# Optimization experiments

Hardware: AMD Instinct MI355X
Metric: run time of the kernel (lower is better)

The kernel has to match this reference:

```python
import jax, jax.numpy as jnp
import numpy as np

B, C_IN, N, K = 4, 128, 2048, 16
DIM, POS, PH, AH = 256, 3, 64, 256 * 4
EPS = 1e-5


def _conv1x1(x, W, b):
    # 1x1 Conv2d: x (B, Cin, n, k) -> (B, Cout, n, k)
    return jnp.einsum('oc,bcnk->bonk', W, x) + b[None, :, None, None]


def _bn(x, gamma, beta, mean, var):
    # eval-mode BatchNorm2d with running stats
    scale = gamma / jnp.sqrt(var + EPS)
    return x * scale[None, :, None, None] + (beta - mean * scale)[None, :, None, None]


def _forward(key, values, pos, Wk, bk, Wq, bq, Wv, bv,
             Wp1, bp1, pg, pb, pm, pv, Wp2, bp2,
             Wa1, ba1, ag, ab, am, av, Wa2, ba2, We, be):
    b, _, n, k = key.shape
    pos_f = jnp.broadcast_to(pos[:, :, :, None], (b, pos.shape[1], n, k))
    kf = _conv1x1(key, Wk, bk)          # (B, dim, n, k)
    v = _conv1x1(values, Wv, bv)        # (B, dim, n, k)
    q = _conv1x1(pos_f, Wq, bq)         # (B, dim, n, k)
    qk_rel = q - kf
    pe = _conv1x1(jax.nn.relu(_bn(_conv1x1(q, Wp1, bp1), pg, pb, pm, pv)), Wp2, bp2)
    attn = _conv1x1(jax.nn.relu(_bn(_conv1x1(qk_rel * pe + pe, Wa1, ba1), ag, ab, am, av)), Wa2, ba2)
    attn = jax.nn.softmax(attn, axis=-1)  # softmax over k neighbors
    agg = jnp.einsum('bcnk,bcnk->bcn', attn, v + pe)  # (B, dim, n)
    return jnp.einsum('oc,bcn->bon', We, agg) + be[None, :, None]


def setup_inputs():
    ks = jax.random.split(jax.random.key(0), 12)
    s = 0.02
    f32 = jnp.float32
    return {
        'key': jax.random.normal(ks[0], (B, C_IN, N, K), f32),
        'values': jax.random.normal(ks[1], (B, C_IN, N, K), f32),
        'pos': jax.random.normal(ks[2], (B, POS, N), f32),
        'Wk': jax.random.normal(ks[3], (DIM, C_IN), f32) * s,
        'bk': jnp.zeros((DIM,), f32),
        'Wq': jax.random.normal(ks[4], (DIM, POS), f32) * s,
        'bq': jnp.zeros((DIM,), f32),
        'Wv': jax.random.normal(ks[5], (DIM, C_IN), f32) * s,
        'bv': jnp.zeros((DIM,), f32),
        'Wp1': jax.random.normal(ks[6], (PH, DIM), f32) * s,
        'bp1': jnp.zeros((PH,), f32),
        'pg': jnp.ones((PH,), f32),
        'pb': jnp.zeros((PH,), f32),
        'pm': jnp.zeros((PH,), f32),
        'pv': jnp.ones((PH,), f32),
        'Wp2': jax.random.normal(ks[7], (DIM, PH), f32) * s,
        'bp2': jnp.zeros((DIM,), f32),
        'Wa1': jax.random.normal(ks[8], (AH, DIM), f32) * s,
        'ba1': jnp.zeros((AH,), f32),
        'ag': jnp.ones((AH,), f32),
        'ab': jnp.zeros((AH,), f32),
        'am': jnp.zeros((AH,), f32),
        'av': jnp.ones((AH,), f32),
        'Wa2': jax.random.normal(ks[9], (DIM, AH), f32) * s,
        'ba2': jnp.zeros((DIM,), f32),
        'We': jax.random.normal(ks[10], (DIM, DIM), f32) * s,
        'be': jnp.zeros((DIM,), f32),
    }


def reference(key, values, pos, Wk, bk, Wq, bq, Wv, bv,
              Wp1, bp1, pg, pb, pm, pv, Wp2, bp2,
              Wa1, ba1, ag, ab, am, av, Wa2, ba2, We, be):
    return _forward(key, values, pos, Wk, bk, Wq, bq, Wv, bv,
                    Wp1, bp1, pg, pb, pm, pv, Wp2, bp2,
                    Wa1, ba1, ag, ab, am, av, Wa2, ba2, We, be)
```

## Files before the change

kernel.cpp:

```cpp
#include <hip/hip_runtime.h>
#include <math.h>

typedef __attribute__((ext_vector_type(8))) short bf16x8;
typedef __attribute__((ext_vector_type(4))) float f32x4;

namespace {
constexpr int NN = 2048;
constexpr float EPSV = 1e-5f;

constexpr size_t WK_O   = 0;
constexpr size_t WV_O   = 65536;
constexpr size_t WEP_O  = 131072;
constexpr size_t B1F_O  = 262144;
constexpr size_t WIMG_O = 266240;
constexpr size_t WP1Q_O = 1314816;
constexpr size_t SC_O   = 1315840;

constexpr int DBUF_OFF = 0;
constexpr int SCW_OFF  = 32768;
constexpr int PE_OFF   = 40960;
constexpr int B1L_OFF  = 49152;
constexpr int LDS_TOTAL = 53248;
}

__device__ __forceinline__ unsigned short f2bf(float x) {
    unsigned u = __float_as_uint(x);
    unsigned r = (u + 0x7FFFu + ((u >> 16) & 1u)) >> 16;
    return (unsigned short)r;
}
__device__ __forceinline__ float bf2f(unsigned short h) {
    return __uint_as_float(((unsigned)h) << 16);
}
__device__ __forceinline__ void gl_lds16(const void* gsrc, void* ldst) {
    __builtin_amdgcn_global_load_lds(
        (const __attribute__((address_space(1))) unsigned int*)gsrc,
        (__attribute__((address_space(3))) unsigned int*)ldst,
        16, 0, 0);
}


__global__ void prep_sc(const float* __restrict__ ag,  const float* __restrict__ ab,
                        const float* __restrict__ am,  const float* __restrict__ av,
                        const float* __restrict__ ba1,
                        const float* __restrict__ Wp1, const float* __restrict__ Wq,
                        const float* __restrict__ bq,  const float* __restrict__ bp1,
                        const float* __restrict__ pg,  const float* __restrict__ pb,
                        const float* __restrict__ pm,  const float* __restrict__ pv,
                        char* __restrict__ ws)
{
    const int t = threadIdx.x, blk = blockIdx.x;
    float* b1f  = (float*)(ws + B1F_O);
    float* sc_s = (float*)(ws + SC_O);
    float* wp1q = (float*)(ws + WP1Q_O);
    if (blk < 4) {
        int j = blk * 256 + t;
        float sc = ag[j] * rsqrtf(av[j] + EPSV);
        sc_s[j] = sc;
        b1f[j] = ba1[j] * sc + ab[j] - am[j] * sc;
    } else if (t < 64) {
        int ph = t;
        float scp = pg[ph] * rsqrtf(pv[ph] + EPSV);
        float a0 = 0.f, a1 = 0.f, a2 = 0.f, abv = 0.f;
        for (int c = 0; c < 256; ++c) {
            float wv = Wp1[ph * 256 + c];
            a0 = fmaf(wv, Wq[c * 3 + 0], a0);
            a1 = fmaf(wv, Wq[c * 3 + 1], a1);
            a2 = fmaf(wv, Wq[c * 3 + 2], a2);
            abv = fmaf(wv, bq[c], abv);
        }
        wp1q[ph * 4 + 0] = scp * a0;
        wp1q[ph * 4 + 1] = scp * a1;
        wp1q[ph * 4 + 2] = scp * a2;
        wp1q[ph * 4 + 3] = scp * (abv + bp1[ph]) + (pb[ph] - pm[ph] * scp);
    }
}

__global__ void prep_cvt(const float* __restrict__ Wk, const float* __restrict__ Wv,
                         const float* __restrict__ We, const float* __restrict__ Wa1,
                         const float* __restrict__ Wa2, char* __restrict__ ws)
{
    const int idx4 = blockIdx.x * 256 + threadIdx.x;
    if (idx4 >= 163840) return;
    const int e0 = idx4 * 4;
    const float* sc_s = (const float*)(ws + SC_O);

    if (e0 < 131072) {
        const float* src;
        unsigned short* dst;
        if (e0 < 32768)      { src = Wk + e0;          dst = (unsigned short*)(ws + WK_O)  + e0; }
        else if (e0 < 65536) { int e = e0 - 32768; src = Wv + e; dst = (unsigned short*)(ws + WV_O)  + e; }
        else                 { int e = e0 - 65536; src = We + e; dst = (unsigned short*)(ws + WEP_O) + e; }
        float4 v = *(const float4*)src;
        ushort4 o;
        o.x = f2bf(v.x); o.y = f2bf(v.y); o.z = f2bf(v.z); o.w = f2bf(v.w);
        *(ushort4*)dst = o;
    } else if (e0 < 393216) {
        int e = e0 - 131072;
        int j = e >> 8, c = e & 255;
        float sc = sc_s[j];
        float4 v = *(const float4*)(Wa1 + e);
        int p = j >> 5, jl = j & 31;
        size_t byte = (size_t)p * 32768 + ((jl * 512 + c * 2) ^ ((jl & 7) << 4));
        ushort4 o;
        o.x = f2bf(v.x * sc); o.y = f2bf(v.y * sc); o.z = f2bf(v.z * sc); o.w = f2bf(v.w * sc);
        *(ushort4*)(ws + WIMG_O + byte) = o;
    } else {
        int e = e0 - 393216;
        int o = e >> 10, j = e & 1023;
        float4 v = *(const float4*)(Wa2 + e);
        int p = j >> 5, jj = j & 31;
        size_t byte = (size_t)p * 32768 + 16384 +
                      (((o >> 1) * 128 + (o & 1) * 64 + jj * 2) ^ (((o >> 1) & 7) << 4));
        ushort4 ov;
        ov.x = f2bf(v.x); ov.y = f2bf(v.y); ov.z = f2bf(v.z); ov.w = f2bf(v.w);
        *(ushort4*)(ws + WIMG_O + byte) = ov;
    }
}

__global__ __launch_bounds__(256) __attribute__((amdgpu_waves_per_eu(2, 2)))
void pt_main(const float* __restrict__ key, const float* __restrict__ values,
             const float* __restrict__ pos,
             const float* __restrict__ Wq,  const float* __restrict__ bq,
             const float* __restrict__ bk,  const float* __restrict__ bv,
             const float* __restrict__ Wp2, const float* __restrict__ bp2,
             const float* __restrict__ be,
             const char* __restrict__ ws,
             float* __restrict__ outp)
{
    extern __shared__ char sm[];
    const int t = threadIdx.x;
    const int w = t >> 6, l = t & 63;
    const int l15 = l & 15, lg = l >> 4;
    const int wg = (blockIdx.x & 7) * 128 + (blockIdx.x >> 3);
    const int b = wg >> 8;
    const int n0 = (wg & 255) * 8;

    char* scw = sm + SCW_OFF + w * 2048;
    char* pew = sm + PE_OFF + w * 2048;
    float* b1l = (float*)(sm + B1L_OFF);

    const unsigned short* wkp = (const unsigned short*)(ws + WK_O);
    const unsigned short* wvp = (const unsigned short*)(ws + WV_O);
    const unsigned short* wep = (const unsigned short*)(ws + WEP_O);
    const float* b1fp = (const float*)(ws + B1F_O);
    const float* wp1q = (const float*)(ws + WP1Q_O);
    const char* wimg = ws + WIMG_O;

    const f32x4 zf = {0.f, 0.f, 0.f, 0.f};

    #pragma unroll
    for (int i = 0; i < 8; ++i)
        gl_lds16(wimg + i * 4096 + t * 16, sm + DBUF_OFF + i * 4096 + t * 16);

    #pragma unroll
    for (int i = 0; i < 4; ++i) b1l[t + i * 256] = b1fp[t + i * 256];

    float p_[2][3];
    {
        const float4 wq4 = *(const float4*)(wp1q + l * 4);
        float h1v[2];
        #pragma unroll
        for (int nl = 0; nl < 2; ++nl) {
            int n = n0 + 2 * w + nl;
            p_[nl][0] = pos[(b * 3 + 0) * NN + n];
            p_[nl][1] = pos[(b * 3 + 1) * NN + n];
            p_[nl][2] = pos[(b * 3 + 2) * NN + n];
            h1v[nl] = fmaxf(fmaf(wq4.x, p_[nl][0],
                            fmaf(wq4.y, p_[nl][1],
                            fmaf(wq4.z, p_[nl][2], wq4.w))), 0.f);
        }
        float pacc[2][4];
        #pragma unroll
        for (int nl = 0; nl < 2; ++nl)
            #pragma unroll
            for (int oi = 0; oi < 4; ++oi) pacc[nl][oi] = 0.f;
        #pragma unroll 4
        for (int j4 = 0; j4 < 16; ++j4) {
            float h0[4], h1[4];
            #pragma unroll
            for (int jj = 0; jj < 4; ++jj) {
                h0[jj] = __shfl(h1v[0], j4 * 4 + jj);
                h1[jj] = __shfl(h1v[1], j4 * 4 + jj);
            }
            #pragma unroll
            for (int oi = 0; oi < 4; ++oi) {
                const float4 wv4 = *(const float4*)(Wp2 + (oi * 64 + l) * 64 + j4 * 4);
                pacc[0][oi] = fmaf(wv4.x, h0[0], fmaf(wv4.y, h0[1], fmaf(wv4.z, h0[2], fmaf(wv4.w, h0[3], pacc[0][oi]))));
                pacc[1][oi] = fmaf(wv4.x, h1[0], fmaf(wv4.y, h1[1], fmaf(wv4.z, h1[2], fmaf(wv4.w, h1[3], pacc[1][oi]))));
            }
        }
        #pragma unroll
        for (int oi = 0; oi < 4; ++oi) {
            int o = oi * 64 + l;
            float bp = bp2[o], bko = bk[o], bqo = bq[o];
            float wq0 = Wq[o * 3 + 0], wq1 = Wq[o * 3 + 1], wq2 = Wq[o * 3 + 2];
            #pragma unroll
            for (int nl = 0; nl < 2; ++nl) {
                float pe = pacc[nl][oi] + bp;
                float q  = fmaf(wq0, p_[nl][0], fmaf(wq1, p_[nl][1], fmaf(wq2, p_[nl][2], bqo)));
                *(unsigned short*)(pew + nl * 512 + o * 2)        = f2bf((q + 1.f - bko) * pe);
                *(unsigned short*)(pew + 1024 + nl * 512 + o * 2) = f2bf(pe);
            }
        }
    }

    const int kq = l & 3, nv = (l >> 2) & 1, c0 = l >> 3;
    f32x4 kacc[2][16];
    #pragma unroll
    for (int mt = 0; mt < 2; ++mt)
        #pragma unroll
        for (int ot = 0; ot < 16; ++ot) kacc[mt][ot] = zf;

    #pragma unroll 1
    for (int s = 0; s < 4; ++s) {
        const float* kb = key + ((size_t)b * 128 * NN + (size_t)(n0 + 2 * w + nv)) * 16 + kq * 4;
        #pragma unroll
        for (int i = 0; i < 4; ++i) {
            int c = s * 32 + i * 8 + c0;
            float4 v = *(const float4*)(kb + (size_t)c * NN * 16);
            int cl = i * 8 + c0;
            #pragma unroll
            for (int j = 0; j < 4; ++j) {
                int m = nv * 16 + kq * 4 + j;
                float fj = (j == 0) ? v.x : (j == 1) ? v.y : (j == 2) ? v.z : v.w;
                *(unsigned short*)(scw + (((m >> 1) * 128 + (m & 1) * 64 + cl * 2) ^ (((m >> 1) & 7) << 4))) = f2bf(fj);
            }
        }
        bf16x8 kB[2];
        #pragma unroll
        for (int mt = 0; mt < 2; ++mt) {
            int m = mt * 16 + l15;
            kB[mt] = *(const bf16x8*)(scw + (((m >> 1) * 128 + (m & 1) * 64 + lg * 16) ^ (((m >> 1) & 7) << 4)));
        }
        #pragma unroll 4
        for (int ot = 0; ot < 16; ++ot) {
            bf16x8 aW = *(const bf16x8*)(wkp + (ot * 16 + l15) * 128 + s * 32 + lg * 8);
            kacc[0][ot] = __builtin_amdgcn_mfma_f32_16x16x32_bf16(aW, kB[0], kacc[0][ot], 0, 0, 0);
            kacc[1][ot] = __builtin_amdgcn_mfma_f32_16x16x32_bf16(aW, kB[1], kacc[1][ot], 0, 0, 0);
        }
    }

    bf16x8 ax[2][8];
    #pragma unroll 1
    for (int x = 0; x < 8; ++x) {
        #pragma unroll
        for (int mt = 0; mt < 2; ++mt) {
            const int m = mt * 16 + l15;
            #pragma unroll
            for (int oi = 0; oi < 2; ++oi) {
                int ot = x * 2 + oi;
                int o0 = ot * 16 + lg * 4;
                ushort4 qv  = *(const ushort4*)(pew + mt * 512 + o0 * 2);
                ushort4 pv4 = *(const ushort4*)(pew + 1024 + mt * 512 + o0 * 2);
                ushort4 pk;
                pk.x = f2bf(bf2f(qv.x) - kacc[mt][ot][0] * bf2f(pv4.x));
                pk.y = f2bf(bf2f(qv.y) - kacc[mt][ot][1] * bf2f(pv4.y));
                pk.z = f2bf(bf2f(qv.z) - kacc[mt][ot][2] * bf2f(pv4.z));
                pk.w = f2bf(bf2f(qv.w) - kacc[mt][ot][3] * bf2f(pv4.w));
                int ol = oi * 16 + lg * 4;
                *(ushort4*)(scw + (((m >> 1) * 128 + (m & 1) * 64 + ol * 2) ^ (((m >> 1) & 7) << 4))) = pk;
            }
        }
        #pragma unroll
        for (int mt = 0; mt < 2; ++mt) {
            int m = mt * 16 + l15;
            ax[mt][x] = *(const bf16x8*)(scw + (((m >> 1) * 128 + (m & 1) * 64 + lg * 16) ^ (((m >> 1) & 7) << 4)));
        }
    }

    f32x4 Y[2][16];
    #pragma unroll
    for (int mt = 0; mt < 2; ++mt)
        #pragma unroll
        for (int ot = 0; ot < 16; ++ot) Y[mt][ot] = zf;

    char* hrb = scw;

    #pragma unroll 1
    for (int p = 0; p < 32; ++p) {
        asm volatile("s_waitcnt vmcnt(0) lgkmcnt(0)" ::: "memory");
        __builtin_amdgcn_s_barrier();
        __builtin_amdgcn_sched_barrier(0);

        __builtin_amdgcn_s_setprio(1);
        #pragma unroll
        for (int jt = 0; jt < 2; ++jt) {
            const int jl = jt * 16 + l15;
            f32x4 c1[2];
            c1[0] = zf; c1[1] = zf;
            #pragma unroll
            for (int kt = 0; kt < 8; ++kt) {
                bf16x8 aw1 = *(const bf16x8*)(sm + DBUF_OFF + jl * 512 + ((kt * 64 + lg * 16) ^ ((jl & 7) << 4)));
                c1[0] = __builtin_amdgcn_mfma_f32_16x16x32_bf16(aw1, ax[0][kt], c1[0], 0, 0, 0);
                c1[1] = __builtin_amdgcn_mfma_f32_16x16x32_bf16(aw1, ax[1][kt], c1[1], 0, 0, 0);
            }
            const float4 b4 = *(const float4*)(b1l + p * 32 + jt * 16 + lg * 4);
            #pragma unroll
            for (int mt = 0; mt < 2; ++mt) {
                int m = mt * 16 + l15;
                ushort4 hw;
                hw.x = f2bf(fmaxf(c1[mt][0] + b4.x, 0.f));
                hw.y = f2bf(fmaxf(c1[mt][1] + b4.y, 0.f));
                hw.z = f2bf(fmaxf(c1[mt][2] + b4.z, 0.f));
                hw.w = f2bf(fmaxf(c1[mt][3] + b4.w, 0.f));
                int jb = (jt * 16 + lg * 4) * 2;
                *(ushort4*)(hrb + (((m >> 1) * 128 + (m & 1) * 64 + jb) ^ (((m >> 1) & 7) << 4))) = hw;
            }
        }
        bf16x8 ah[2];
        #pragma unroll
        for (int mt = 0; mt < 2; ++mt) {
            int m = mt * 16 + l15;
            ah[mt] = *(const bf16x8*)(hrb + (((m >> 1) * 128 + (m & 1) * 64 + lg * 16) ^ (((m >> 1) & 7) << 4)));
        }
        #pragma unroll
        for (int ot = 0; ot < 16; ++ot) {
            int o = ot * 16 + l15;
            bf16x8 bW2 = *(const bf16x8*)(sm + DBUF_OFF + 16384 +
                          (((o >> 1) * 128 + (o & 1) * 64 + lg * 16) ^ (((o >> 1) & 7) << 4)));
            Y[0][ot] = __builtin_amdgcn_mfma_f32_16x16x32_bf16(ah[0], bW2, Y[0][ot], 0, 0, 0);
            Y[1][ot] = __builtin_amdgcn_mfma_f32_16x16x32_bf16(ah[1], bW2, Y[1][ot], 0, 0, 0);
        }
        __builtin_amdgcn_s_setprio(0);

        asm volatile("s_waitcnt lgkmcnt(0)" ::: "memory");
        __builtin_amdgcn_s_barrier();
        if (p < 31) {
            const char* src = wimg + (size_t)(p + 1) * 32768;
            #pragma unroll
            for (int i = 0; i < 8; ++i)
                gl_lds16(src + i * 4096 + t * 16, sm + DBUF_OFF + i * 4096 + t * 16);
        }
    }

    #pragma unroll
    for (int mt = 0; mt < 2; ++mt) {
        #pragma unroll
        for (int ot = 0; ot < 16; ++ot) {
            float mx = fmaxf(fmaxf(Y[mt][ot][0], Y[mt][ot][1]), fmaxf(Y[mt][ot][2], Y[mt][ot][3]));
            mx = fmaxf(mx, __shfl_xor(mx, 16));
            mx = fmaxf(mx, __shfl_xor(mx, 32));
            float e0 = expf(Y[mt][ot][0] - mx), e1 = expf(Y[mt][ot][1] - mx);
            float e2 = expf(Y[mt][ot][2] - mx), e3 = expf(Y[mt][ot][3] - mx);
            float s = e0 + e1 + e2 + e3;
            s += __shfl_xor(s, 16);
            s += __shfl_xor(s, 32);
            float inv = 1.f / s;
            Y[mt][ot][0] = e0 * inv; Y[mt][ot][1] = e1 * inv;
            Y[mt][ot][2] = e2 * inv; Y[mt][ot][3] = e3 * inv;
        }
    }

    bf16x8 vB[2][4];
    #pragma unroll 1
    for (int s = 0; s < 4; ++s) {
        const float* vb = values + ((size_t)b * 128 * NN + (size_t)(n0 + 2 * w + nv)) * 16 + kq * 4;
        #pragma unroll
        for (int i = 0; i < 4; ++i) {
            int c = s * 32 + i * 8 + c0;
            float4 v = *(const float4*)(vb + (size_t)c * NN * 16);
            int cl = i * 8 + c0;
            #pragma unroll
            for (int j = 0; j < 4; ++j) {
                int m = nv * 16 + kq * 4 + j;
                float fj = (j == 0) ? v.x : (j == 1) ? v.y : (j == 2) ? v.z : v.w;
                *(unsigned short*)(scw + (((m >> 1) * 128 + (m & 1) * 64 + cl * 2) ^ (((m >> 1) & 7) << 4))) = f2bf(fj);
            }
        }
        #pragma unroll
        for (int mt = 0; mt < 2; ++mt) {
            int m = mt * 16 + l15;
            vB[mt][s] = *(const bf16x8*)(scw + (((m >> 1) * 128 + (m & 1) * 64 + lg * 16) ^ (((m >> 1) & 7) << 4)));
        }
    }

    float aggv[2][16];
    #pragma unroll 4
    for (int ot = 0; ot < 16; ++ot) {
        int o = ot * 16 + l15;
        f32x4 v0 = zf, v1 = zf;
        #pragma unroll
        for (int s = 0; s < 4; ++s) {
            bf16x8 bWv = *(const bf16x8*)(wvp + o * 128 + s * 32 + lg * 8);
            v0 = __builtin_amdgcn_mfma_f32_16x16x32_bf16(vB[0][s], bWv, v0, 0, 0, 0);
            v1 = __builtin_amdgcn_mfma_f32_16x16x32_bf16(vB[1][s], bWv, v1, 0, 0, 0);
        }
        float bvo = bv[o];
        #pragma unroll
        for (int mt = 0; mt < 2; ++mt) {
            f32x4 va = mt ? v1 : v0;
            float s = Y[mt][ot][0] * (va[0] + bvo);
            s = fmaf(Y[mt][ot][1], va[1] + bvo, s);
            s = fmaf(Y[mt][ot][2], va[2] + bvo, s);
            s = fmaf(Y[mt][ot][3], va[3] + bvo, s);
            s += __shfl_xor(s, 16);
            s += __shfl_xor(s, 32);
            aggv[mt][ot] = s + bf2f(*(const unsigned short*)(pew + 1024 + mt * 512 + o * 2));
        }
    }

    __syncthreads();
    if (lg == 0) {
        #pragma unroll
        for (int mt = 0; mt < 2; ++mt) {
            int nl = 2 * w + mt;
            #pragma unroll
            for (int ot = 0; ot < 16; ++ot) {
                int o = ot * 16 + l15;
                *(unsigned short*)(sm + PE_OFF + ((nl * 512 + o * 2) ^ ((nl & 7) << 4))) = f2bf(aggv[mt][ot]);
            }
        }
    }
    __syncthreads();

    bf16x8 aa[8];
    #pragma unroll
    for (int kt = 0; kt < 8; ++kt)
        aa[kt] = *(const bf16x8*)(sm + PE_OFF + ((l15 * 512 + kt * 64 + lg * 16) ^ ((l15 & 7) << 4)));
    #pragma unroll
    for (int ot = 0; ot < 4; ++ot) {
        int oo = w * 64 + ot * 16 + l15;
        f32x4 acc = zf;
        #pragma unroll
        for (int kt = 0; kt < 8; ++kt) {
            bf16x8 bWe = *(const bf16x8*)(wep + oo * 256 + kt * 32 + lg * 8);
            acc = __builtin_amdgcn_mfma_f32_16x16x32_bf16(aa[kt], bWe, acc, 0, 0, 0);
        }
        if (lg < 2) {
            float bev = be[oo];
            float4 vv;
            vv.x = acc[0] + bev; vv.y = acc[1] + bev;
            vv.z = acc[2] + bev; vv.w = acc[3] + bev;
            *(float4*)(outp + ((size_t)(b * 256 + oo)) * NN + n0 + lg * 4) = vv;
        }
    }
}

extern "C" void kernel_launch(void* const* d_in, const int* in_sizes, int n_in,
                              void* d_out, int out_size, void* d_ws, size_t ws_size,
                              hipStream_t stream) {
    const float* key    = (const float*)d_in[0];
    const float* values = (const float*)d_in[1];
    const float* pos    = (const float*)d_in[2];
    const float* Wk     = (const float*)d_in[3];
    const float* bk     = (const float*)d_in[4];
    const float* Wq     = (const float*)d_in[5];
    const float* bq     = (const float*)d_in[6];
    const float* Wv     = (const float*)d_in[7];
    const float* bv     = (const float*)d_in[8];
    const float* Wp1    = (const float*)d_in[9];
    const float* bp1    = (const float*)d_in[10];
    const float* pg     = (const float*)d_in[11];
    const float* pb     = (const float*)d_in[12];
    const float* pm     = (const float*)d_in[13];
    const float* pv     = (const float*)d_in[14];
    const float* Wp2    = (const float*)d_in[15];
    const float* bp2    = (const float*)d_in[16];
    const float* Wa1    = (const float*)d_in[17];
    const float* ba1    = (const float*)d_in[18];
    const float* ag     = (const float*)d_in[19];
    const float* ab     = (const float*)d_in[20];
    const float* am     = (const float*)d_in[21];
    const float* av     = (const float*)d_in[22];
    const float* Wa2    = (const float*)d_in[23];
    const float* We     = (const float*)d_in[25];
    const float* be     = (const float*)d_in[26];
    (void)in_sizes; (void)n_in; (void)out_size; (void)ws_size;

    char* ws = (char*)d_ws;

    hipFuncSetAttribute((const void*)pt_main,
                        hipFuncAttributeMaxDynamicSharedMemorySize, LDS_TOTAL);

    hipLaunchKernelGGL(prep_sc, dim3(5), dim3(256), 0, stream,
                       ag, ab, am, av, ba1, Wp1, Wq, bq, bp1, pg, pb, pm, pv, ws);
    hipLaunchKernelGGL(prep_cvt, dim3(640), dim3(256), 0, stream,
                       Wk, Wv, We, Wa1, Wa2, ws);
    hipLaunchKernelGGL(pt_main, dim3(1024), dim3(256), LDS_TOTAL, stream,
                       key, values, pos, Wq, bq, bk, bv, Wp2, bp2, be,
                       (const char*)ws, (float*)d_out);
}
```

Baseline: 589.6 us.

## Halve points per wave to cut registers and raise occupancy to three blocks

Each wave now handles one point instead of two, so the per-wave accumulators (kacc, Y, ax, vB) are halved and the grid doubles to 2048 blocks of 4 points each. LDS per block shrinks and launch bounds move from a fixed 2 waves/EU to a minimum of 3 blocks per CU, to gain latency hiding. The cost is that each weight fragment (Wk, Wa1, Wa2, Wv, We) loaded from LDS or global now feeds half as many MFMAs, which doubles weight traffic per point and doubles the per-block weight image load. The final We GEMM also uses only a quarter of its 16-wide M tile.

```diff
diff --git a/kernel.cpp b/kernel.cpp
--- a/kernel.cpp
+++ b/kernel.cpp
@@ -18,9 +18,9 @@
 
 constexpr int DBUF_OFF = 0;
 constexpr int SCW_OFF  = 32768;
-constexpr int PE_OFF   = 40960;
-constexpr int B1L_OFF  = 49152;
-constexpr int LDS_TOTAL = 53248;
+constexpr int PE_OFF   = 36864;
+constexpr int B1L_OFF  = 40960;
+constexpr int LDS_TOTAL = 45056;
 }
 
 __device__ __forceinline__ unsigned short f2bf(float x) {
@@ -117,7 +117,7 @@
     }
 }
 
-__global__ __launch_bounds__(256) __attribute__((amdgpu_waves_per_eu(2, 2)))
+__global__ __launch_bounds__(256, 3)
 void pt_main(const float* __restrict__ key, const float* __restrict__ values,
              const float* __restrict__ pos,
              const float* __restrict__ Wq,  const float* __restrict__ bq,
@@ -131,12 +131,13 @@
     const int t = threadIdx.x;
     const int w = t >> 6, l = t & 63;
     const int l15 = l & 15, lg = l >> 4;
-    const int wg = (blockIdx.x & 7) * 128 + (blockIdx.x >> 3);
-    const int b = wg >> 8;
-    const int n0 = (wg & 255) * 8;
-
-    char* scw = sm + SCW_OFF + w * 2048;
-    char* pew = sm + PE_OFF + w * 2048;
+    const int wg = (blockIdx.x & 7) * 256 + (blockIdx.x >> 3);
+    const int b = wg >> 9;
+    const int n0 = (wg & 511) * 4;
+    const int n = n0 + w;
+
+    char* scw = sm + SCW_OFF + w * 1024;
+    char* pew = sm + PE_OFF + w * 1024;
     float* b1l = (float*)(sm + B1L_OFF);
 
     const unsigned short* wkp = (const unsigned short*)(ws + WK_O);
@@ -155,124 +156,88 @@
     #pragma unroll
     for (int i = 0; i < 4; ++i) b1l[t + i * 256] = b1fp[t + i * 256];
 
-    float p_[2][3];
+    float p0, p1, p2;
     {
         const float4 wq4 = *(const float4*)(wp1q + l * 4);
-        float h1v[2];
-        #pragma unroll
-        for (int nl = 0; nl < 2; ++nl) {
-            int n = n0 + 2 * w + nl;
-            p_[nl][0] = pos[(b * 3 + 0) * NN + n];
-            p_[nl][1] = pos[(b * 3 + 1) * NN + n];
-            p_[nl][2] = pos[(b * 3 + 2) * NN + n];
-            h1v[nl] = fmaxf(fmaf(wq4.x, p_[nl][0],
-                            fmaf(wq4.y, p_[nl][1],
-                            fmaf(wq4.z, p_[nl][2], wq4.w))), 0.f);
-        }
-        float pacc[2][4];
-        #pragma unroll
-        for (int nl = 0; nl < 2; ++nl)
-            #pragma unroll
-            for (int oi = 0; oi < 4; ++oi) pacc[nl][oi] = 0.f;
+        p0 = pos[(b * 3 + 0) * NN + n];
+        p1 = pos[(b * 3 + 1) * NN + n];
+        p2 = pos[(b * 3 + 2) * NN + n];
+        float h1v = fmaxf(fmaf(wq4.x, p0, fmaf(wq4.y, p1, fmaf(wq4.z, p2, wq4.w))), 0.f);
+        float pacc[4];
+        #pragma unroll
+        for (int oi = 0; oi < 4; ++oi) pacc[oi] = 0.f;
         #pragma unroll 4
         for (int j4 = 0; j4 < 16; ++j4) {
-            float h0[4], h1[4];
-            #pragma unroll
-            for (int jj = 0; jj < 4; ++jj) {
-                h0[jj] = __shfl(h1v[0], j4 * 4 + jj);
-                h1[jj] = __shfl(h1v[1], j4 * 4 + jj);
-            }
+            float h[4];
+            #pragma unroll
+            for (int jj = 0; jj < 4; ++jj) h[jj] = __shfl(h1v, j4 * 4 + jj);
             #pragma unroll
             for (int oi = 0; oi < 4; ++oi) {
                 const float4 wv4 = *(const float4*)(Wp2 + (oi * 64 + l) * 64 + j4 * 4);
-                pacc[0][oi] = fmaf(wv4.x, h0[0], fmaf(wv4.y, h0[1], fmaf(wv4.z, h0[2], fmaf(wv4.w, h0[3], pacc[0][oi]))));
-                pacc[1][oi] = fmaf(wv4.x, h1[0], fmaf(wv4.y, h1[1], fmaf(wv4.z, h1[2], fmaf(wv4.w, h1[3], pacc[1][oi]))));
+                pacc[oi] = fmaf(wv4.x, h[0], fmaf(wv4.y, h[1], fmaf(wv4.z, h[2], fmaf(wv4.w, h[3], pacc[oi]))));
             }
         }
         #pragma unroll
         for (int oi = 0; oi < 4; ++oi) {
             int o = oi * 64 + l;
-            float bp = bp2[o], bko = bk[o], bqo = bq[o];
-            float wq0 = Wq[o * 3 + 0], wq1 = Wq[o * 3 + 1], wq2 = Wq[o * 3 + 2];
-            #pragma unroll
-            for (int nl = 0; nl < 2; ++nl) {
-                float pe = pacc[nl][oi] + bp;
-                float q  = fmaf(wq0, p_[nl][0], fmaf(wq1, p_[nl][1], fmaf(wq2, p_[nl][2], bqo)));
-                *(unsigned short*)(pew + nl * 512 + o * 2)        = f2bf((q + 1.f - bko) * pe);
-                *(unsigned short*)(pew + 1024 + nl * 512 + o * 2) = f2bf(pe);
-            }
-        }
-    }
-
-    const int kq = l & 3, nv = (l >> 2) & 1, c0 = l >> 3;
-    f32x4 kacc[2][16];
-    #pragma unroll
-    for (int mt = 0; mt < 2; ++mt)
-        #pragma unroll
-        for (int ot = 0; ot < 16; ++ot) kacc[mt][ot] = zf;
+            float pe = pacc[oi] + bp2[o];
+            float q  = fmaf(Wq[o * 3 + 0], p0, fmaf(Wq[o * 3 + 1], p1, fmaf(Wq[o * 3 + 2], p2, bq[o])));
+            *(unsigned short*)(pew + o * 2)       = f2bf((q + 1.f - bk[o]) * pe);
+            *(unsigned short*)(pew + 512 + o * 2) = f2bf(pe);
+        }
+    }
+
+    const int kq = l & 3, cL = l >> 2;
+    f32x4 kacc[16];
+    #pragma unroll
+    for (int ot = 0; ot < 16; ++ot) kacc[ot] = zf;
 
     #pragma unroll 1
     for (int s = 0; s < 4; ++s) {
-        const float* kb = key + ((size_t)b * 128 * NN + (size_t)(n0 + 2 * w + nv)) * 16 + kq * 4;
-        #pragma unroll
-        for (int i = 0; i < 4; ++i) {
-            int c = s * 32 + i * 8 + c0;
+        const float* kb = key + ((size_t)b * 128 * NN + n) * 16 + kq * 4;
+        #pragma unroll
+        for (int h = 0; h < 2; ++h) {
+            int c = s * 32 + h * 16 + cL;
             float4 v = *(const float4*)(kb + (size_t)c * NN * 16);
-            int cl = i * 8 + c0;
+            int cl = h * 16 + cL;
             #pragma unroll
             for (int j = 0; j < 4; ++j) {
-                int m = nv * 16 + kq * 4 + j;
+                int m = kq * 4 + j;
                 float fj = (j == 0) ? v.x : (j == 1) ? v.y : (j == 2) ? v.z : v.w;
                 *(unsigned short*)(scw + (((m >> 1) * 128 + (m & 1) * 64 + cl * 2) ^ (((m >> 1) & 7) << 4))) = f2bf(fj);
             }
         }
-        bf16x8 kB[2];
-        #pragma unroll
-        for (int mt = 0; mt < 2; ++mt) {
-            int m = mt * 16 + l15;
-            kB[mt] = *(const bf16x8*)(scw + (((m >> 1) * 128 + (m & 1) * 64 + lg * 16) ^ (((m >> 1) & 7) << 4)));
-        }
+        bf16x8 kB = *(const bf16x8*)(scw + (((l15 >> 1) * 128 + (l15 & 1) * 64 + lg * 16) ^ (((l15 >> 1) & 7) << 4)));
         #pragma unroll 4
         for (int ot = 0; ot < 16; ++ot) {
             bf16x8 aW = *(const bf16x8*)(wkp + (ot * 16 + l15) * 128 + s * 32 + lg * 8);
-            kacc[0][ot] = __builtin_amdgcn_mfma_f32_16x16x32_bf16(aW, kB[0], kacc[0][ot], 0, 0, 0);
-            kacc[1][ot] = __builtin_amdgcn_mfma_f32_16x16x32_bf16(aW, kB[1], kacc[1][ot], 0, 0, 0);
-        }
-    }
-
-    bf16x8 ax[2][8];
+            kacc[ot] = __builtin_amdgcn_mfma_f32_16x16x32_bf16(aW, kB, kacc[ot], 0, 0, 0);
+        }
+    }
+
+    bf16x8 ax[8];
     #pragma unroll 1
     for (int x = 0; x < 8; ++x) {
         #pragma unroll
-        for (int mt = 0; mt < 2; ++mt) {
-            const int m = mt * 16 + l15;
-            #pragma unroll
-            for (int oi = 0; oi < 2; ++oi) {
-                int ot = x * 2 + oi;
-                int o0 = ot * 16 + lg * 4;
-                ushort4 qv  = *(const ushort4*)(pew + mt * 512 + o0 * 2);
-                ushort4 pv4 = *(const ushort4*)(pew + 1024 + mt * 512 + o0 * 2);
-                ushort4 pk;
-                pk.x = f2bf(bf2f(qv.x) - kacc[mt][ot][0] * bf2f(pv4.x));
-                pk.y = f2bf(bf2f(qv.y) - kacc[mt][ot][1] * bf2f(pv4.y));
-                pk.z = f2bf(bf2f(qv.z) - kacc[mt][ot][2] * bf2f(pv4.z));
-                pk.w = f2bf(bf2f(qv.w) - kacc[mt][ot][3] * bf2f(pv4.w));
-                int ol = oi * 16 + lg * 4;
-                *(ushort4*)(scw + (((m >> 1) * 128 + (m & 1) * 64 + ol * 2) ^ (((m >> 1) & 7) << 4))) = pk;
-            }
-        }
-        #pragma unroll
-        for (int mt = 0; mt < 2; ++mt) {
-            int m = mt * 16 + l15;
-            ax[mt][x] = *(const bf16x8*)(scw + (((m >> 1) * 128 + (m & 1) * 64 + lg * 16) ^ (((m >> 1) & 7) << 4)));
-        }
-    }
-
-    f32x4 Y[2][16];
-    #pragma unroll
-    for (int mt = 0; mt < 2; ++mt)
-        #pragma unroll
-        for (int ot = 0; ot < 16; ++ot) Y[mt][ot] = zf;
+        for (int oi = 0; oi < 2; ++oi) {
+            int ot = x * 2 + oi;
+            int o0 = ot * 16 + lg * 4;
+            ushort4 qv  = *(const ushort4*)(pew + o0 * 2);
+            ushort4 pv4 = *(const ushort4*)(pew + 512 + o0 * 2);
+            ushort4 pk;
+            pk.x = f2bf(bf2f(qv.x) - kacc[ot][0] * bf2f(pv4.x));
+            pk.y = f2bf(bf2f(qv.y) - kacc[ot][1] * bf2f(pv4.y));
+            pk.z = f2bf(bf2f(qv.z) - kacc[ot][2] * bf2f(pv4.z));
+            pk.w = f2bf(bf2f(qv.w) - kacc[ot][3] * bf2f(pv4.w));
+            int ol = oi * 16 + lg * 4;
+            *(ushort4*)(scw + (((l15 >> 1) * 128 + (l15 & 1) * 64 + ol * 2) ^ (((l15 >> 1) & 7) << 4))) = pk;
+        }
+        ax[x] = *(const bf16x8*)(scw + (((l15 >> 1) * 128 + (l15 & 1) * 64 + lg * 16) ^ (((l15 >> 1) & 7) << 4)));
+    }
+
+    f32x4 Y[16];
+    #pragma unroll
+    for (int ot = 0; ot < 16; ++ot) Y[ot] = zf;
 
     char* hrb = scw;
 
@@ -286,40 +251,28 @@
         #pragma unroll
         for (int jt = 0; jt < 2; ++jt) {
             const int jl = jt * 16 + l15;
-            f32x4 c1[2];
-            c1[0] = zf; c1[1] = zf;
+            f32x4 c1 = zf;
             #pragma unroll
             for (int kt = 0; kt < 8; ++kt) {
                 bf16x8 aw1 = *(const bf16x8*)(sm + DBUF_OFF + jl * 512 + ((kt * 64 + lg * 16) ^ ((jl & 7) << 4)));
-                c1[0] = __builtin_amdgcn_mfma_f32_16x16x32_bf16(aw1, ax[0][kt], c1[0], 0, 0, 0);
-                c1[1] = __builtin_amdgcn_mfma_f32_16x16x32_bf16(aw1, ax[1][kt], c1[1], 0, 0, 0);
+                c1 = __builtin_amdgcn_mfma_f32_16x16x32_bf16(aw1, ax[kt], c1, 0, 0, 0);
             }
             const float4 b4 = *(const float4*)(b1l + p * 32 + jt * 16 + lg * 4);
-            #pragma unroll
-            for (int mt = 0; mt < 2; ++mt) {
-                int m = mt * 16 + l15;
-                ushort4 hw;
-                hw.x = f2bf(fmaxf(c1[mt][0] + b4.x, 0.f));
-                hw.y = f2bf(fmaxf(c1[mt][1] + b4.y, 0.f));
-                hw.z = f2bf(fmaxf(c1[mt][2] + b4.z, 0.f));
-                hw.w = f2bf(fmaxf(c1[mt][3] + b4.w, 0.f));
-                int jb = (jt * 16 + lg * 4) * 2;
-                *(ushort4*)(hrb + (((m >> 1) * 128 + (m & 1) * 64 + jb) ^ (((m >> 1) & 7) << 4))) = hw;
-            }
-        }
-        bf16x8 ah[2];
-        #pragma unroll
-        for (int mt = 0; mt < 2; ++mt) {
-            int m = mt * 16 + l15;
-            ah[mt] = *(const bf16x8*)(hrb + (((m >> 1) * 128 + (m & 1) * 64 + lg * 16) ^ (((m >> 1) & 7) << 4)));
-        }
+            ushort4 hw;
+            hw.x = f2bf(fmaxf(c1[0] + b4.x, 0.f));
+            hw.y = f2bf(fmaxf(c1[1] + b4.y, 0.f));
+            hw.z = f2bf(fmaxf(c1[2] + b4.z, 0.f));
+            hw.w = f2bf(fmaxf(c1[3] + b4.w, 0.f));
+            int jb = (jt * 16 + lg * 4) * 2;
+            *(ushort4*)(hrb + (((l15 >> 1) * 128 + (l15 & 1) * 64 + jb) ^ (((l15 >> 1) & 7) << 4))) = hw;
+        }
+        bf16x8 ah = *(const bf16x8*)(hrb + (((l15 >> 1) * 128 + (l15 & 1) * 64 + lg * 16) ^ (((l15 >> 1) & 7) << 4)));
         #pragma unroll
         for (int ot = 0; ot < 16; ++ot) {
             int o = ot * 16 + l15;
             bf16x8 bW2 = *(const bf16x8*)(sm + DBUF_OFF + 16384 +
                           (((o >> 1) * 128 + (o & 1) * 64 + lg * 16) ^ (((o >> 1) & 7) << 4)));
-            Y[0][ot] = __builtin_amdgcn_mfma_f32_16x16x32_bf16(ah[0], bW2, Y[0][ot], 0, 0, 0);
-            Y[1][ot] = __builtin_amdgcn_mfma_f32_16x16x32_bf16(ah[1], bW2, Y[1][ot], 0, 0, 0);
+            Y[ot] = __builtin_amdgcn_mfma_f32_16x16x32_bf16(ah, bW2, Y[ot], 0, 0, 0);
         }
         __builtin_amdgcn_s_setprio(0);
 
@@ -334,81 +287,65 @@
     }
 
     #pragma unroll
-    for (int mt = 0; mt < 2; ++mt) {
-        #pragma unroll
-        for (int ot = 0; ot < 16; ++ot) {
-            float mx = fmaxf(fmaxf(Y[mt][ot][0], Y[mt][ot][1]), fmaxf(Y[mt][ot][2], Y[mt][ot][3]));
-            mx = fmaxf(mx, __shfl_xor(mx, 16));
-            mx = fmaxf(mx, __shfl_xor(mx, 32));
-            float e0 = expf(Y[mt][ot][0] - mx), e1 = expf(Y[mt][ot][1] - mx);
-            float e2 = expf(Y[mt][ot][2] - mx), e3 = expf(Y[mt][ot][3] - mx);
-            float s = e0 + e1 + e2 + e3;
-            s += __shfl_xor(s, 16);
-            s += __shfl_xor(s, 32);
-            float inv = 1.f / s;
-            Y[mt][ot][0] = e0 * inv; Y[mt][ot][1] = e1 * inv;
-            Y[mt][ot][2] = e2 * inv; Y[mt][ot][3] = e3 * inv;
-        }
-    }
-
-    bf16x8 vB[2][4];
+    for (int ot = 0; ot < 16; ++ot) {
+        float mx = fmaxf(fmaxf(Y[ot][0], Y[ot][1]), fmaxf(Y[ot][2], Y[ot][3]));
+        mx = fmaxf(mx, __shfl_xor(mx, 16));
+        mx = fmaxf(mx, __shfl_xor(mx, 32));
+        float e0 = expf(Y[ot][0] - mx), e1 = expf(Y[ot][1] - mx);
+        float e2 = expf(Y[ot][2] - mx), e3 = expf(Y[ot][3] - mx);
+        float s = e0 + e1 + e2 + e3;
+        s += __shfl_xor(s, 16);
+        s += __shfl_xor(s, 32);
+        float inv = 1.f / s;
+        Y[ot][0] = e0 * inv; Y[ot][1] = e1 * inv;
+        Y[ot][2] = e2 * inv; Y[ot][3] = e3 * inv;
+    }
+
+    bf16x8 vB[4];
     #pragma unroll 1
     for (int s = 0; s < 4; ++s) {
-        const float* vb = values + ((size_t)b * 128 * NN + (size_t)(n0 + 2 * w + nv)) * 16 + kq * 4;
-        #pragma unroll
-        for (int i = 0; i < 4; ++i) {
-            int c = s * 32 + i * 8 + c0;
+        const float* vb = values + ((size_t)b * 128 * NN + n) * 16 + kq * 4;
+        #pragma unroll
+        for (int h = 0; h < 2; ++h) {
+            int c = s * 32 + h * 16 + cL;
             float4 v = *(const float4*)(vb + (size_t)c * NN * 16);
-            int cl = i * 8 + c0;
+            int cl = h * 16 + cL;
             #pragma unroll
             for (int j = 0; j < 4; ++j) {
-                int m = nv * 16 + kq * 4 + j;
+                int m = kq * 4 + j;
                 float fj = (j == 0) ? v.x : (j == 1) ? v.y : (j == 2) ? v.z : v.w;
                 *(unsigned short*)(scw + (((m >> 1) * 128 + (m & 1) * 64 + cl * 2) ^ (((m >> 1) & 7) << 4))) = f2bf(fj);
             }
         }
-        #pragma unroll
-        for (int mt = 0; mt < 2; ++mt) {
-            int m = mt * 16 + l15;
-            vB[mt][s] = *(const bf16x8*)(scw + (((m >> 1) * 128 + (m & 1) * 64 + lg * 16) ^ (((m >> 1) & 7) << 4)));
-        }
-    }
-
-    float aggv[2][16];
+        vB[s] = *(const bf16x8*)(scw + (((l15 >> 1) * 128 + (l15 & 1) * 64 + lg * 16) ^ (((l15 >> 1) & 7) << 4)));
+    }
+
+    float aggv[16];
     #pragma unroll 4
     for (int ot = 0; ot < 16; ++ot) {
         int o = ot * 16 + l15;
-        f32x4 v0 = zf, v1 = zf;
+        f32x4 va = zf;
         #pragma unroll
         for (int s = 0; s < 4; ++s) {
             bf16x8 bWv = *(const bf16x8*)(wvp + o * 128 + s * 32 + lg * 8);
-            v0 = __builtin_amdgcn_mfma_f32_16x16x32_bf16(vB[0][s], bWv, v0, 0, 0, 0);
-            v1 = __builtin_amdgcn_mfma_f32_16x16x32_bf16(vB[1][s], bWv, v1, 0, 0, 0);
+            va = __builtin_amdgcn_mfma_f32_16x16x32_bf16(vB[s], bWv, va, 0, 0, 0);
         }
         float bvo = bv[o];
-        #pragma unroll
-        for (int mt = 0; mt < 2; ++mt) {
-            f32x4 va = mt ? v1 : v0;
-            float s = Y[mt][ot][0] * (va[0] + bvo);
-            s = fmaf(Y[mt][ot][1], va[1] + bvo, s);
-            s = fmaf(Y[mt][ot][2], va[2] + bvo, s);
-            s = fmaf(Y[mt][ot][3], va[3] + bvo, s);
-            s += __shfl_xor(s, 16);
-            s += __shfl_xor(s, 32);
-            aggv[mt][ot] = s + bf2f(*(const unsigned short*)(pew + 1024 + mt * 512 + o * 2));
-        }
+        float s = Y[ot][0] * (va[0] + bvo);
+        s = fmaf(Y[ot][1], va[1] + bvo, s);
+        s = fmaf(Y[ot][2], va[2] + bvo, s);
+        s = fmaf(Y[ot][3], va[3] + bvo, s);
+        s += __shfl_xor(s, 16);
+        s += __shfl_xor(s, 32);
+        aggv[ot] = s + bf2f(*(const unsigned short*)(pew + 512 + o * 2));
     }
 
     __syncthreads();
     if (lg == 0) {
         #pragma unroll
-        for (int mt = 0; mt < 2; ++mt) {
-            int nl = 2 * w + mt;
-            #pragma unroll
-            for (int ot = 0; ot < 16; ++ot) {
-                int o = ot * 16 + l15;
-                *(unsigned short*)(sm + PE_OFF + ((nl * 512 + o * 2) ^ ((nl & 7) << 4))) = f2bf(aggv[mt][ot]);
-            }
+        for (int ot = 0; ot < 16; ++ot) {
+            int o = ot * 16 + l15;
+            *(unsigned short*)(sm + PE_OFF + ((w * 512 + o * 2) ^ ((w & 7) << 4))) = f2bf(aggv[ot]);
         }
     }
     __syncthreads();
@@ -426,12 +363,12 @@
             bf16x8 bWe = *(const bf16x8*)(wep + oo * 256 + kt * 32 + lg * 8);
             acc = __builtin_amdgcn_mfma_f32_16x16x32_bf16(aa[kt], bWe, acc, 0, 0, 0);
         }
-        if (lg < 2) {
+        if (lg == 0) {
             float bev = be[oo];
             float4 vv;
             vv.x = acc[0] + bev; vv.y = acc[1] + bev;
             vv.z = acc[2] + bev; vv.w = acc[3] + bev;
-            *(float4*)(outp + ((size_t)(b * 256 + oo)) * NN + n0 + lg * 4) = vv;
+            *(float4*)(outp + ((size_t)(b * 256 + oo)) * NN + n0) = vv;
         }
     }
 }
@@ -476,7 +413,7 @@
                        ag, ab, am, av, ba1, Wp1, Wq, bq, bp1, pg, pb, pm, pv, ws);
     hipLaunchKernelGGL(prep_cvt, dim3(640), dim3(256), 0, stream,
                        Wk, Wv, We, Wa1, Wa2, ws);
-    hipLaunchKernelGGL(pt_main, dim3(1024), dim3(256), LDS_TOTAL, stream,
+    hipLaunchKernelGGL(pt_main, dim3(2048), dim3(256), LDS_TOTAL, stream,
                        key, values, pos, Wq, bq, bk, bv, Wp2, bp2, be,
                        (const char*)ws, (float*)d_out);
 }
```

New measurement: 612.5 us. 3.9% more time.
